# Kernel optimization log

Measured on AMD Instinct MI355X. Metric: run time of the kernel, lower is better.

The kernel has to match this reference:

```python
import jax, jax.numpy as jnp
import numpy as np

N_NODES = 10000
N_EDGES = 80000
OBS_DIMS = 128
HIDDEN = 1024
ACT_DIMS = 8
N_GRAPHS = 64


def setup_inputs() -> dict:
    key = jax.random.key(0)
    ks = jax.random.split(key, 8)
    x = jax.random.normal(ks[0], (N_NODES, OBS_DIMS), dtype=jnp.float32)
    edge_index = jax.random.randint(ks[1], (2, N_EDGES), 0, N_NODES, dtype=jnp.int64)
    batch = jnp.sort(jax.random.randint(ks[2], (N_NODES,), 0, N_GRAPHS, dtype=jnp.int64))
    # Glorot-style init for weights, zero bias (as in PyG GCNConv / Linear defaults)
    W1 = jax.random.normal(ks[3], (OBS_DIMS, HIDDEN), dtype=jnp.float32) * (1.0 / np.sqrt(OBS_DIMS))
    b1 = jnp.zeros((HIDDEN,), dtype=jnp.float32)
    W2 = jax.random.normal(ks[4], (HIDDEN, HIDDEN), dtype=jnp.float32) * (1.0 / np.sqrt(HIDDEN))
    b2 = jnp.zeros((HIDDEN,), dtype=jnp.float32)
    Wl = jax.random.normal(ks[5], (HIDDEN, ACT_DIMS), dtype=jnp.float32) * (1.0 / np.sqrt(HIDDEN))
    bl = jnp.zeros((ACT_DIMS,), dtype=jnp.float32)
    return {"x": x, "edge_index": edge_index, "batch": batch,
            "W1": W1, "b1": b1, "W2": W2, "b2": b2, "Wl": Wl, "bl": bl}


def _gcn_conv(x, src, dst, dinv, W, b, n):
    """PyG GCNConv: D^-1/2 (A+I) D^-1/2 X W + b (self-loops already in src/dst)."""
    h = x @ W                                   # [N, out]
    norm = (dinv[src] * dinv[dst])[:, None]      # [E+N, 1]
    msg = h[src] * norm                          # gather + scale
    out = jax.ops.segment_sum(msg, dst, num_segments=n)
    return out + b


def reference(x, edge_index, batch, W1, b1, W2, b2, Wl, bl):
    n = x.shape[0]
    loops = jnp.arange(n, dtype=edge_index.dtype)
    src = jnp.concatenate([edge_index[0], loops])  # add self-loops
    dst = jnp.concatenate([edge_index[1], loops])
    # degree (with self-loops) from destination column, as PyG does
    deg = jax.ops.segment_sum(jnp.ones_like(dst, dtype=x.dtype), dst, num_segments=n)
    dinv = jax.lax.rsqrt(jnp.maximum(deg, 1.0))

    h = jax.nn.relu(_gcn_conv(x, src, dst, dinv, W1, b1, n))
    h = _gcn_conv(h, src, dst, dinv, W2, b2, n)
    h = jnp.tanh(h @ Wl + bl)                    # [N, act_dims]

    # global_mean_pool over batch segment ids
    sums = jax.ops.segment_sum(h, batch, num_segments=N_GRAPHS)
    counts = jax.ops.segment_sum(jnp.ones((n, 1), h.dtype), batch, num_segments=N_GRAPHS)
    return sums / jnp.maximum(counts, 1.0)       # [N_GRAPHS, act_dims]
```

## Files before the change

kernel.cpp:

```cpp
#include <hip/hip_runtime.h>
#include <hip/hip_bf16.h>

#define NNODES 10000
#define NEDGES 80000
#define OBS    128
#define HID    1024
#define ACTD   8
#define NGR    64

typedef __bf16 bf16x8 __attribute__((ext_vector_type(8)));
typedef float  f32x4  __attribute__((ext_vector_type(4)));
typedef const __attribute__((address_space(1))) unsigned int gl_u32;
typedef __attribute__((address_space(3))) unsigned int lds_u32;

__device__ __forceinline__ ushort f2b(float f) {
    union { float f; unsigned int i; } v; v.f = f;
    unsigned int lsb = (v.i >> 16) & 1u;
    unsigned int r = v.i + 0x7fffu + lsb;
    return (ushort)(r >> 16);
}
__device__ __forceinline__ int cix(int v, int hi) {
    return v < 0 ? 0 : (v >= hi ? hi - 1 : v);
}

__global__ __launch_bounds__(256) void k_prep(const float* __restrict__ W1,
                                              const float* __restrict__ W2,
                                              const float* __restrict__ Wl,
                                              const float* __restrict__ b2,
                                              const float* __restrict__ bl,
                                              ushort* __restrict__ Wt1,
                                              ushort* __restrict__ M2bf,
                                              float* __restrict__ b2l,
                                              float* __restrict__ zacc,
                                              float* __restrict__ pool,
                                              float* __restrict__ cnt,
                                              int* __restrict__ degi) {
    int blk = blockIdx.x;
    if (blk >= 385) {
        int idx = (blk - 385) * 256 + threadIdx.x;
        if (idx < NNODES * ACTD) zacc[idx] = 0.0f;
        if (idx < NGR * ACTD) pool[idx] = 0.0f;
        if (idx < NGR) cnt[idx] = 0.0f;
        if (idx < NNODES) degi[idx] = 0;
        return;
    }
    if (blk < 128) {
        __shared__ float tile[32][33];
        int bx = (blk & 31) * 32, by = (blk >> 5) * 32;
        int tx = threadIdx.x & 31, ty = threadIdx.x >> 5;
        #pragma unroll
        for (int i = 0; i < 32; i += 8)
            tile[ty + i][tx] = W1[(size_t)(by + ty + i) * HID + bx + tx];
        __syncthreads();
        #pragma unroll
        for (int i = 0; i < 32; i += 8)
            Wt1[(size_t)(bx + ty + i) * OBS + by + tx] = f2b(tile[tx][ty + i]);
        return;
    }
    int wvid = ((blk - 128) * 256 + (int)threadIdx.x) >> 6;
    int lane = threadIdx.x & 63;
    if (wvid > HID) return;
    const float* row = (wvid == HID) ? b2 : (W2 + (size_t)wvid * HID);
    float acc[ACTD];
    #pragma unroll
    for (int j = 0; j < ACTD; ++j) acc[j] = 0.0f;
    for (int it = 0; it < HID / 64; ++it) {
        int k = it * 64 + lane;
        float w2v = row[k];
        float4 a = *(const float4*)(Wl + (size_t)k * ACTD);
        float4 b = *(const float4*)(Wl + (size_t)k * ACTD + 4);
        acc[0] += w2v * a.x; acc[1] += w2v * a.y; acc[2] += w2v * a.z; acc[3] += w2v * a.w;
        acc[4] += w2v * b.x; acc[5] += w2v * b.y; acc[6] += w2v * b.z; acc[7] += w2v * b.w;
    }
    #pragma unroll
    for (int off = 32; off > 0; off >>= 1)
        #pragma unroll
        for (int j = 0; j < ACTD; ++j)
            acc[j] += __shfl_down(acc[j], off);
    if (lane == 0) {
        if (wvid == HID) {
            #pragma unroll
            for (int j = 0; j < ACTD; ++j) b2l[j] = acc[j] + bl[j];
        } else {
            #pragma unroll
            for (int j = 0; j < ACTD; ++j) M2bf[wvid * ACTD + j] = f2b(acc[j]);
        }
    }
}

__global__ void k_count(const int* __restrict__ dst, int* degi, int e) {
    int i = blockIdx.x * 256 + threadIdx.x;
    if (i < e) atomicAdd(&degi[cix(dst[i], NNODES)], 1);
}

__global__ __launch_bounds__(1024) void k_scan(const int* __restrict__ degi,
                                               int* rowptr, int* cursor, float* dinv) {
    __shared__ int wsum[16];
    int t = threadIdx.x, lane = t & 63, w = t >> 6;
    int base = t * 10;
    int local[10];
    int s = 0;
    #pragma unroll
    for (int k = 0; k < 10; ++k) {
        int i = base + k;
        int v = 0;
        if (i < NNODES) {
            v = degi[i];
            dinv[i] = rsqrtf((float)(v + 1));
        }
        local[k] = s; s += v;
    }
    int sc = s;
    #pragma unroll
    for (int off = 1; off < 64; off <<= 1) {
        int u = __shfl_up(sc, off);
        if (lane >= off) sc += u;
    }
    if (lane == 63) wsum[w] = sc;
    __syncthreads();
    if (w == 0 && lane < 16) {
        int v = wsum[lane];
        #pragma unroll
        for (int off = 1; off < 16; off <<= 1) {
            int u = __shfl_up(v, off);
            if (lane >= off) v += u;
        }
        wsum[lane] = v;
    }
    __syncthreads();
    int excl = ((w == 0) ? 0 : wsum[w - 1]) + (sc - s);
    #pragma unroll
    for (int k = 0; k < 10; ++k) {
        int i = base + k;
        if (i < NNODES) { rowptr[i] = excl + local[k]; cursor[i] = excl + local[k]; }
    }
    if (t == 0) rowptr[NNODES] = wsum[15];
}

__global__ void k_fill(const int* __restrict__ src, const int* __restrict__ dst,
                       const float* __restrict__ dinv, int* cursor,
                       int* __restrict__ esrc, float* __restrict__ coefs, int e) {
    int i = blockIdx.x * 256 + threadIdx.x;
    if (i >= e) return;
    int s = cix(src[i], NNODES), d = cix(dst[i], NNODES);
    int pos = atomicAdd(&cursor[d], 1);
    esrc[pos] = s;
    coefs[pos] = dinv[s] * dinv[d];
}

__global__ void k_aggx(const float* __restrict__ x, const float* __restrict__ dinv,
                       const int* __restrict__ rowptr, const int* __restrict__ esrc,
                       const float* __restrict__ coefs, ushort* __restrict__ aggbf, int n) {
    int wv = (blockIdx.x * 256 + threadIdx.x) >> 6;
    int lane = threadIdx.x & 63;
    if (wv >= n) return;
    int half = lane >> 5, c = lane & 31;
    float d = dinv[wv];
    float4 v = make_float4(0.f, 0.f, 0.f, 0.f);
    if (half == 0) {
        float d2 = d * d;
        float4 xs = *(const float4*)(x + (size_t)wv * OBS + c * 4);
        v.x = xs.x * d2; v.y = xs.y * d2; v.z = xs.z * d2; v.w = xs.w * d2;
    }
    int e1 = rowptr[wv + 1];
    for (int e = rowptr[wv] + half; e < e1; e += 2) {
        int s = esrc[e];
        float cf = coefs[e];
        float4 a = *(const float4*)(x + (size_t)s * OBS + c * 4);
        v.x += a.x * cf; v.y += a.y * cf; v.z += a.z * cf; v.w += a.w * cf;
    }
    v.x += __shfl_down(v.x, 32);
    v.y += __shfl_down(v.y, 32);
    v.z += __shfl_down(v.z, 32);
    v.w += __shfl_down(v.w, 32);
    if (half == 0) {
        ushort4 o;
        o.x = f2b(v.x); o.y = f2b(v.y); o.z = f2b(v.z); o.w = f2b(v.w);
        *(ushort4*)(aggbf + (size_t)wv * OBS + c * 4) = o;
    }
}

__global__ __launch_bounds__(256) void k_gemm1_fused(const ushort* __restrict__ A,
                                                     const ushort* __restrict__ Bt,
                                                     const float* __restrict__ bias,
                                                     const ushort* __restrict__ M2bf,
                                                     float* __restrict__ zacc,
                                                     int M) {
    __shared__ ushort buf[128 * 136 + 16 * 128];
    ushort* As    = buf;
    ushort* Bs    = buf + 8192;
    ushort* stage = buf;
    ushort* M2t   = buf + 128 * 136;

    const int t = threadIdx.x;
    const int bm = blockIdx.x, bn = blockIdx.y;
    const int lane = t & 63, wv = t >> 6;
    const int wm = (wv & 1) * 64, wn = (wv >> 1) * 64;
    const int l16 = lane & 15, kg = (lane >> 4) * 8;

    if (t < 128) {
        ushort4 a = *(const ushort4*)(M2bf + (size_t)(bn * 128 + t) * ACTD);
        ushort4 b = *(const ushort4*)(M2bf + (size_t)(bn * 128 + t) * ACTD + 4);
        M2t[0 * 128 + t] = a.x; M2t[1 * 128 + t] = a.y;
        M2t[2 * 128 + t] = a.z; M2t[3 * 128 + t] = a.w;
        M2t[4 * 128 + t] = b.x; M2t[5 * 128 + t] = b.y;
        M2t[6 * 128 + t] = b.z; M2t[7 * 128 + t] = b.w;
        #pragma unroll
        for (int j = 8; j < 16; ++j) M2t[j * 128 + t] = 0;
    }

    f32x4 acc[4][4];
    #pragma unroll
    for (int i = 0; i < 4; ++i)
        #pragma unroll
        for (int j = 0; j < 4; ++j)
            acc[i][j] = (f32x4){0.f, 0.f, 0.f, 0.f};

    const int rs = t >> 3;
    const int cs = (t & 7) * 8;
    #pragma unroll
    for (int kt = 0; kt < OBS; kt += 64) {
        #pragma unroll
        for (int p = 0; p < 4; ++p) {
            int r = rs + p * 32;
            int gr = bm * 128 + r; if (gr >= M) gr = M - 1;
            __builtin_amdgcn_global_load_lds(
                (gl_u32*)(A + (size_t)gr * OBS + kt + cs),
                (lds_u32*)(As + r * 64 + cs), 16, 0, 0);
            int gn = bn * 128 + r;
            __builtin_amdgcn_global_load_lds(
                (gl_u32*)(Bt + (size_t)gn * OBS + kt + cs),
                (lds_u32*)(Bs + r * 64 + cs), 16, 0, 0);
        }
        __syncthreads();
        #pragma unroll
        for (int k2 = 0; k2 < 64; k2 += 32) {
            bf16x8 af[4], bfr[4];
            #pragma unroll
            for (int i = 0; i < 4; ++i)
                af[i] = *(const bf16x8*)(As + (wm + i * 16 + l16) * 64 + k2 + kg);
            #pragma unroll
            for (int j = 0; j < 4; ++j)
                bfr[j] = *(const bf16x8*)(Bs + (wn + j * 16 + l16) * 64 + k2 + kg);
            #pragma unroll
            for (int i = 0; i < 4; ++i)
                #pragma unroll
                for (int j = 0; j < 4; ++j)
                    acc[i][j] = __builtin_amdgcn_mfma_f32_16x16x32_bf16(af[i], bfr[j], acc[i][j], 0, 0, 0);
        }
        __syncthreads();
    }

    #pragma unroll
    for (int i = 0; i < 4; ++i) {
        int rowb = wm + i * 16 + (lane >> 4) * 4;
        #pragma unroll
        for (int j = 0; j < 4; ++j) {
            int col = wn + j * 16 + l16;
            float bj = bias[bn * 128 + col];
            #pragma unroll
            for (int r = 0; r < 4; ++r)
                stage[(rowb + r) * 136 + col] = f2b(fmaxf(acc[i][j][r] + bj, 0.0f));
        }
    }
    __syncthreads();

    #pragma unroll
    for (int st = 0; st < 2; ++st) {
        int row0 = wv * 32 + st * 16;
        f32x4 z = (f32x4){0.f, 0.f, 0.f, 0.f};
        #pragma unroll
        for (int kt = 0; kt < 128; kt += 32) {
            bf16x8 a = *(const bf16x8*)(stage + (row0 + l16) * 136 + kt + kg);
            bf16x8 b = *(const bf16x8*)(M2t + l16 * 128 + kt + kg);
            z = __builtin_amdgcn_mfma_f32_16x16x32_bf16(a, b, z, 0, 0, 0);
        }
        if (l16 < ACTD) {
            int rowb = bm * 128 + row0 + (lane >> 4) * 4;
            #pragma unroll
            for (int r = 0; r < 4; ++r)
                if (rowb + r < M)
                    atomicAdd(&zacc[(size_t)(rowb + r) * ACTD + l16], z[r]);
        }
    }
}

__global__ __launch_bounds__(1024) void k_zfinal(const float* __restrict__ zacc,
                                                 const float* __restrict__ dinv,
                                                 const int* __restrict__ rowptr,
                                                 const int* __restrict__ esrc,
                                                 const float* __restrict__ coefs,
                                                 const float* __restrict__ b2l,
                                                 const int* __restrict__ batch,
                                                 float* __restrict__ pool,
                                                 float* __restrict__ cnt, int n) {
    __shared__ float part[NGR * ACTD];
    __shared__ int   partc[NGR];
    int t = threadIdx.x;
    if (t < NGR * ACTD) part[t] = 0.0f;
    if (t < NGR) partc[t] = 0;
    __syncthreads();

    int idx = blockIdx.x * 1024 + t;
    int i = idx >> 3, j = idx & 7;
    if (i < n) {
        float d = dinv[i];
        float v = zacc[idx] * d * d;
        int e0 = rowptr[i], e1 = rowptr[i + 1];
        for (int e = e0; e < e1; ++e)
            v += coefs[e] * zacc[(size_t)esrc[e] * ACTD + j];
        float tz = tanhf(v + b2l[j]);
        int g = cix(batch[i], NGR);
        atomicAdd(&part[g * ACTD + j], tz);
        if (j == 0) atomicAdd(&partc[g], 1);
    }
    __syncthreads();

    int i0 = (blockIdx.x * 1024) >> 3;
    int i1 = (blockIdx.x * 1024 + 1023) >> 3;
    if (i0 >= n) return;
    if (i1 >= n) i1 = n - 1;
    int g0 = cix(batch[i0], NGR), g1 = cix(batch[i1], NGR);
    int ng = g1 - g0 + 1;
    if (t < ng * ACTD)
        atomicAdd(&pool[g0 * ACTD + t], part[g0 * ACTD + t]);
    if (t < ng) {
        int c = partc[g0 + t];
        if (c) atomicAdd(&cnt[g0 + t], (float)c);
    }
}

__global__ void k_final(const float* __restrict__ pool, const float* __restrict__ cnt,
                        float* __restrict__ out, int total) {
    int i = blockIdx.x * 256 + threadIdx.x;
    if (i < total) out[i] = pool[i] / fmaxf(cnt[i >> 3], 1.0f);
}

extern "C" void kernel_launch(void* const* d_in, const int* in_sizes, int n_in,
                              void* d_out, int out_size, void* d_ws, size_t ws_size,
                              hipStream_t stream) {
    const float* x   = (const float*)d_in[0];
    const int*   ei  = (const int*)d_in[1];
    const int*   bat = (const int*)d_in[2];
    const float* W1  = (const float*)d_in[3];
    const float* b1  = (const float*)d_in[4];
    const float* W2  = (const float*)d_in[5];
    const float* b2v = (const float*)d_in[6];
    const float* Wl  = (const float*)d_in[7];
    const float* bl  = (const float*)d_in[8];
    float* out = (float*)d_out;

    const int N = NNODES, E = NEDGES;
    const int* src = ei;
    const int* dst = ei + E;

    char* ws = (char*)d_ws;
    size_t off = 0;
    float*  pool   = (float*)(ws + off); off += 2048;
    float*  cnt    = (float*)(ws + off); off += 256;
    float*  dinv   = (float*)(ws + off); off += 40192;
    int*    degi   = (int*)(ws + off);   off += 40192;
    int*    rowptr = (int*)(ws + off);   off += 40448;
    int*    cursor = (int*)(ws + off);   off += 40192;
    int*    esrc   = (int*)(ws + off);   off += (size_t)E * 4;
    float*  coefs  = (float*)(ws + off); off += (size_t)E * 4;
    float*  b2l    = (float*)(ws + off); off += 256;
    ushort* M2bf   = (ushort*)(ws + off); off += (size_t)HID * ACTD * 2;
    ushort* Wt1    = (ushort*)(ws + off); off += (size_t)HID * OBS * 2;
    float*  zacc   = (float*)(ws + off); off += (size_t)N * ACTD * 4;
    ushort* aggbf  = (ushort*)(ws + off); off += (size_t)N * OBS * 2;

    k_prep<<<698, 256, 0, stream>>>(W1, W2, Wl, b2v, bl, Wt1, M2bf, b2l,
                                    zacc, pool, cnt, degi);
    k_count<<<(E + 255) / 256, 256, 0, stream>>>(dst, degi, E);
    k_scan<<<1, 1024, 0, stream>>>(degi, rowptr, cursor, dinv);
    k_fill<<<(E + 255) / 256, 256, 0, stream>>>(src, dst, dinv, cursor, esrc, coefs, E);

    k_aggx<<<(N * 64 + 255) / 256, 256, 0, stream>>>(x, dinv, rowptr, esrc, coefs, aggbf, N);

    k_gemm1_fused<<<dim3((N + 127) / 128, HID / 128), 256, 0, stream>>>(
        aggbf, Wt1, b1, M2bf, zacc, N);

    k_zfinal<<<(N * ACTD + 1023) / 1024, 1024, 0, stream>>>(
        zacc, dinv, rowptr, esrc, coefs, b2l, bat, pool, cnt, N);
    k_final<<<2, 256, 0, stream>>>(pool, cnt, out, NGR * ACTD);
}
```

Measured before the change: 133.8 us.

## Prefetch x into cache during degree count, widen aggregation lanes, shrink zfinal blocks

Result: no change. 132.5 us (-1.0%).

```diff
diff --git a/kernel.cpp b/kernel.cpp
--- a/kernel.cpp
+++ b/kernel.cpp
@@ -10,6 +10,7 @@
 
 typedef __bf16 bf16x8 __attribute__((ext_vector_type(8)));
 typedef float  f32x4  __attribute__((ext_vector_type(4)));
+typedef ushort us8    __attribute__((ext_vector_type(8)));
 typedef const __attribute__((address_space(1))) unsigned int gl_u32;
 typedef __attribute__((address_space(3))) unsigned int lds_u32;
 
@@ -88,9 +89,17 @@
     }
 }
 
-__global__ void k_count(const int* __restrict__ dst, int* degi, int e) {
+__global__ void k_count(const int* __restrict__ dst, int* degi,
+                        const float* __restrict__ xw, int e) {
     int i = blockIdx.x * 256 + threadIdx.x;
     if (i < e) atomicAdd(&degi[cix(dst[i], NNODES)], 1);
+    float wacc = 0.0f;
+    int stride = gridDim.x * 256;
+    for (int k = i; k < NNODES * OBS / 4; k += stride) {
+        float4 v = *((const float4*)xw + k);
+        wacc += v.x + v.y + v.z + v.w;
+    }
+    asm volatile("" :: "v"(wacc));
 }
 
 __global__ __launch_bounds__(1024) void k_scan(const int* __restrict__ degi,
@@ -154,29 +163,38 @@
     int wv = (blockIdx.x * 256 + threadIdx.x) >> 6;
     int lane = threadIdx.x & 63;
     if (wv >= n) return;
-    int half = lane >> 5, c = lane & 31;
-    float d = dinv[wv];
-    float4 v = make_float4(0.f, 0.f, 0.f, 0.f);
-    if (half == 0) {
-        float d2 = d * d;
-        float4 xs = *(const float4*)(x + (size_t)wv * OBS + c * 4);
-        v.x = xs.x * d2; v.y = xs.y * d2; v.z = xs.z * d2; v.w = xs.w * d2;
+    int q = lane >> 4, c = lane & 15;
+    float4 v0 = make_float4(0.f, 0.f, 0.f, 0.f), v1 = v0;
+    if (q == 0) {
+        float d = dinv[wv], d2 = d * d;
+        const float* xs = x + (size_t)wv * OBS + c * 8;
+        float4 a0 = *(const float4*)(xs);
+        float4 a1 = *(const float4*)(xs + 4);
+        v0.x = a0.x * d2; v0.y = a0.y * d2; v0.z = a0.z * d2; v0.w = a0.w * d2;
+        v1.x = a1.x * d2; v1.y = a1.y * d2; v1.z = a1.z * d2; v1.w = a1.w * d2;
     }
     int e1 = rowptr[wv + 1];
-    for (int e = rowptr[wv] + half; e < e1; e += 2) {
+    for (int e = rowptr[wv] + q; e < e1; e += 4) {
         int s = esrc[e];
         float cf = coefs[e];
-        float4 a = *(const float4*)(x + (size_t)s * OBS + c * 4);
-        v.x += a.x * cf; v.y += a.y * cf; v.z += a.z * cf; v.w += a.w * cf;
-    }
-    v.x += __shfl_down(v.x, 32);
-    v.y += __shfl_down(v.y, 32);
-    v.z += __shfl_down(v.z, 32);
-    v.w += __shfl_down(v.w, 32);
-    if (half == 0) {
-        ushort4 o;
-        o.x = f2b(v.x); o.y = f2b(v.y); o.z = f2b(v.z); o.w = f2b(v.w);
-        *(ushort4*)(aggbf + (size_t)wv * OBS + c * 4) = o;
+        const float* xs = x + (size_t)s * OBS + c * 8;
+        float4 a0 = *(const float4*)(xs);
+        float4 a1 = *(const float4*)(xs + 4);
+        v0.x += a0.x * cf; v0.y += a0.y * cf; v0.z += a0.z * cf; v0.w += a0.w * cf;
+        v1.x += a1.x * cf; v1.y += a1.y * cf; v1.z += a1.z * cf; v1.w += a1.w * cf;
+    }
+    #pragma unroll
+    for (int off = 16; off <= 32; off <<= 1) {
+        v0.x += __shfl_xor(v0.x, off); v0.y += __shfl_xor(v0.y, off);
+        v0.z += __shfl_xor(v0.z, off); v0.w += __shfl_xor(v0.w, off);
+        v1.x += __shfl_xor(v1.x, off); v1.y += __shfl_xor(v1.y, off);
+        v1.z += __shfl_xor(v1.z, off); v1.w += __shfl_xor(v1.w, off);
+    }
+    if (q == 0) {
+        us8 o;
+        o[0] = f2b(v0.x); o[1] = f2b(v0.y); o[2] = f2b(v0.z); o[3] = f2b(v0.w);
+        o[4] = f2b(v1.x); o[5] = f2b(v1.y); o[6] = f2b(v1.z); o[7] = f2b(v1.w);
+        *(us8*)(aggbf + (size_t)wv * OBS + c * 8) = o;
     }
 }
 
@@ -285,23 +303,23 @@
     }
 }
 
-__global__ __launch_bounds__(1024) void k_zfinal(const float* __restrict__ zacc,
-                                                 const float* __restrict__ dinv,
-                                                 const int* __restrict__ rowptr,
-                                                 const int* __restrict__ esrc,
-                                                 const float* __restrict__ coefs,
-                                                 const float* __restrict__ b2l,
-                                                 const int* __restrict__ batch,
-                                                 float* __restrict__ pool,
-                                                 float* __restrict__ cnt, int n) {
+__global__ __launch_bounds__(256) void k_zfinal(const float* __restrict__ zacc,
+                                                const float* __restrict__ dinv,
+                                                const int* __restrict__ rowptr,
+                                                const int* __restrict__ esrc,
+                                                const float* __restrict__ coefs,
+                                                const float* __restrict__ b2l,
+                                                const int* __restrict__ batch,
+                                                float* __restrict__ pool,
+                                                float* __restrict__ cnt, int n) {
     __shared__ float part[NGR * ACTD];
     __shared__ int   partc[NGR];
     int t = threadIdx.x;
-    if (t < NGR * ACTD) part[t] = 0.0f;
+    part[t] = 0.0f; part[t + 256] = 0.0f;
     if (t < NGR) partc[t] = 0;
     __syncthreads();
 
-    int idx = blockIdx.x * 1024 + t;
+    int idx = blockIdx.x * 256 + t;
     int i = idx >> 3, j = idx & 7;
     if (i < n) {
         float d = dinv[i];
@@ -316,17 +334,17 @@
     }
     __syncthreads();
 
-    int i0 = (blockIdx.x * 1024) >> 3;
-    int i1 = (blockIdx.x * 1024 + 1023) >> 3;
+    int i0 = (blockIdx.x * 256) >> 3;
+    int i1 = (blockIdx.x * 256 + 255) >> 3;
     if (i0 >= n) return;
     if (i1 >= n) i1 = n - 1;
     int g0 = cix(batch[i0], NGR), g1 = cix(batch[i1], NGR);
     int ng = g1 - g0 + 1;
-    if (t < ng * ACTD)
-        atomicAdd(&pool[g0 * ACTD + t], part[g0 * ACTD + t]);
-    if (t < ng) {
-        int c = partc[g0 + t];
-        if (c) atomicAdd(&cnt[g0 + t], (float)c);
+    for (int u = t; u < ng * ACTD; u += 256)
+        atomicAdd(&pool[g0 * ACTD + u], part[g0 * ACTD + u]);
+    for (int u = t; u < ng; u += 256) {
+        int c = partc[g0 + u];
+        if (c) atomicAdd(&cnt[g0 + u], (float)c);
     }
 }
 
@@ -372,7 +390,7 @@
 
     k_prep<<<698, 256, 0, stream>>>(W1, W2, Wl, b2v, bl, Wt1, M2bf, b2l,
                                     zacc, pool, cnt, degi);
-    k_count<<<(E + 255) / 256, 256, 0, stream>>>(dst, degi, E);
+    k_count<<<(E + 255) / 256, 256, 0, stream>>>(dst, degi, x, E);
     k_scan<<<1, 1024, 0, stream>>>(degi, rowptr, cursor, dinv);
     k_fill<<<(E + 255) / 256, 256, 0, stream>>>(src, dst, dinv, cursor, esrc, coefs, E);
 
@@ -381,7 +399,7 @@
     k_gemm1_fused<<<dim3((N + 127) / 128, HID / 128), 256, 0, stream>>>(
         aggbf, Wt1, b1, M2bf, zacc, N);
 
-    k_zfinal<<<(N * ACTD + 1023) / 1024, 1024, 0, stream>>>(
+    k_zfinal<<<(N * ACTD + 255) / 256, 256, 0, stream>>>(
         zacc, dinv, rowptr, esrc, coefs, b2l, bat, pool, cnt, N);
     k_final<<<2, 256, 0, stream>>>(pool, cnt, out, NGR * ACTD);
 }
```
